# Kernel tuning notes

Measured on AMD Instinct MI355X. Metric: run time of the kernel, lower is better.

Reference implementation:

```python
import jax, jax.numpy as jnp
import numpy as np

# Hyperparameters (DetectionLoss __init__ defaults)
ALPHA = 0.75
GAMMA = 2.0
NUM_NEG = 10000
NUM_HARD = 100
NEG_POS_RATIO = 100
FN_WEIGHT = 4.0
FN_THRESHOLD = 0.8
HFP_T1 = 0.5
HFP_T2 = 0.7
HFP_W1 = 1.5
HFP_W2 = 2.0

B, N = 16, 884736  # batch, num anchor points (96^3 crop)


def setup_inputs() -> dict:
    key = jax.random.key(0)
    kp, kt, km = jax.random.split(key, 3)
    pred = jax.random.normal(kp, (B, N, 1), dtype=jnp.float32)
    # sparse binary positive targets (~440 positives per sample)
    target = (jax.random.uniform(kt, (B, N, 1)) < 5e-4).astype(jnp.float32)
    mask_ignore = (jax.random.uniform(km, (B, N, 1)) < 1e-2).astype(jnp.float32)
    mask_ignore = mask_ignore * (1.0 - target)
    return {"pred": pred, "target": target, "mask_ignore": mask_ignore}


def _bce_with_logits(x, t):
    # numerically stable binary_cross_entropy_with_logits, reduction='none'
    return jnp.maximum(x, 0.0) - x * t + jnp.log1p(jnp.exp(-jnp.abs(x)))


def _cls_loss(pred, target, mask_ignore):
    b = pred.shape[0]
    pred = pred.reshape(b, -1)
    target = target.reshape(b, -1)
    mask_ignore = mask_ignore.reshape(b, -1)
    # fixed keys replace python random.sample for negative subsampling
    keys = jax.random.split(jax.random.key(42), b)

    def per_sample(pred_b, target_b, mask_b, key):
        is_pos = target_b == 1.0
        is_neg = target_b == 0.0
        cls_prob = jnp.clip(jax.nn.sigmoid(jax.lax.stop_gradient(pred_b)), 1e-4, 1.0 - 1e-4)
        alpha_factor = jnp.where(is_pos, ALPHA, 1.0 - ALPHA)
        focal_w = alpha_factor * jnp.where(is_pos, 1.0 - cls_prob, cls_prob) ** GAMMA
        loss = jnp.where(mask_b == 0.0, focal_w * _bce_with_logits(pred_b, target_b), 0.0)
        npos = jnp.sum(is_pos)
        # false-negative upweight (only positive points qualify, so it is a
        # no-op in the npos==0 branch, matching the torch control flow)
        loss = loss * jnp.where((cls_prob < FN_THRESHOLD) & is_pos, FN_WEIGHT, 1.0)
        # hard false-positive upweight (applied in both branches)
        hfp_w = HFP_W1 + jnp.clip((cls_prob - HFP_T1) / (HFP_T2 - HFP_T1), 0.0, 1.0) * (HFP_W2 - HFP_W1)
        loss = loss * jnp.where((cls_prob > HFP_T1) & is_neg, hfp_w, 1.0)
        pos_loss = jnp.sum(jnp.where(is_pos, loss, 0.0))
        # random subsample of NUM_NEG negatives without replacement:
        # top-NUM_NEG by uniform random score restricted to negatives
        rnd = jax.random.uniform(key, pred_b.shape)
        sample_score = jnp.where(is_neg, rnd, -jnp.inf)
        _, idx = jax.lax.top_k(sample_score, NUM_NEG)
        neg_losses = jnp.where(is_neg[idx], loss[idx], 0.0)
        # hard-negative mining: keep top-k of the sampled negative losses
        topv = jax.lax.top_k(neg_losses, NUM_NEG)[0]
        k = jnp.where(npos > 0, jnp.minimum(NEG_POS_RATIO * npos, NUM_NEG), NUM_HARD)
        neg_sum = jnp.sum(jnp.where(jnp.arange(NUM_NEG) < k, topv, 0.0))
        # pos branch divides both sums by npos; neg branch divides by 1
        denom = jnp.where(npos > 0, jnp.maximum(npos.astype(pred_b.dtype), 1.0), 1.0)
        return pos_loss / denom, neg_sum / denom

    pos, neg = jax.vmap(per_sample)(pred, target, mask_ignore, keys)
    cls_pos_loss = jnp.sum(pos) / b
    cls_neg_loss = jnp.sum(neg) / b
    return jnp.stack([cls_pos_loss, cls_neg_loss])


def reference(pred, target, mask_ignore):
    return _cls_loss(pred, target, mask_ignore)
```

## Files before the change

kernel.cpp:

```cpp
#include <hip/hip_runtime.h>
#include <stdint.h>


#define BATCH 16
#define NPTS 884736u
#define THRESH_KEY 8266976u
#define THRESH_W   4232691712u
#define KEYMAX 8388607u
#define KSEL 10000u
#define TLO 8285746u
#define THI 8301746u
#define TLO_W 4242301952u
#define HI_W  4250494464u
#define WCAP 3072u
#define SCAP 160
#define BCAP 64
#define NBLK 432u
#define EPT 8u
#define HDRB 512


struct KeyPairs { unsigned k[2 * BATCH]; };

__host__ __device__ __forceinline__ void tf2x32(unsigned k0, unsigned k1,
                                                unsigned x0, unsigned x1,
                                                unsigned& o0, unsigned& o1)
{
  unsigned ks0 = k0, ks1 = k1, ks2 = k0 ^ k1 ^ 0x1BD11BDAu;
  x0 += ks0; x1 += ks1;
#define TF_R(r) { x0 += x1; x1 = __builtin_rotateleft32(x1, r); x1 ^= x0; }
  TF_R(13) TF_R(15) TF_R(26) TF_R(6)
  x0 += ks1; x1 += ks2 + 1u;
  TF_R(17) TF_R(29) TF_R(16) TF_R(24)
  x0 += ks2; x1 += ks0 + 2u;
  TF_R(13) TF_R(15) TF_R(26) TF_R(6)
  x0 += ks0; x1 += ks1 + 3u;
  TF_R(17) TF_R(29) TF_R(16) TF_R(24)
  x0 += ks1; x1 += ks2 + 4u;
  TF_R(13) TF_R(15) TF_R(26) TF_R(6)
  x0 += ks2; x1 += ks0 + 5u;
#undef TF_R
  o0 = x0; o1 = x1;
}

__device__ __forceinline__ float lossf(float x, float t, float m)
{
  float e  = __expf(-x);
  float p  = __fdividef(1.0f, 1.0f + e);
  p = fminf(fmaxf(p, 1e-4f), 1.0f - 1e-4f);
  bool is_pos = (t == 1.0f);
  float alpha = is_pos ? 0.75f : 0.25f;
  float pw = is_pos ? (1.0f - p) : p;
  float soft = __logf(1.0f + __expf(-fabsf(x)));
  float bce = fmaxf(x, 0.0f) - x * t + soft;
  float L = (m == 0.0f) ? alpha * pw * pw * bce : 0.0f;
  if (is_pos && p < 0.8f) L *= 4.0f;
  if (!is_pos && p > 0.5f)
    L *= 1.5f + fminf(fmaxf((p - 0.5f) * 5.0f, 0.0f), 1.0f) * 0.5f;
  return L;
}

__global__ __launch_bounds__(256) void mono(
    const float* __restrict__ pred, const float* __restrict__ target,
    const float* __restrict__ mask, char* __restrict__ hdr,
    unsigned* __restrict__ wkey, unsigned* __restrict__ widx,
    float* __restrict__ wloss, KeyPairs kp)
{
  const int b = blockIdx.y;
  const int tid = threadIdx.x;
  const unsigned i0 = (blockIdx.x * 256u + tid) * EPT;
  const size_t sbase = (size_t)b * NPTS;
  const size_t off = sbase + i0;
  const unsigned k0 = kp.k[2 * b], k1 = kp.k[2 * b + 1];
  char* line = hdr + (size_t)b * HDRB;

  __shared__ unsigned s_n, s_nhi, s_npos;
  __shared__ float    s_psum, s_hsum;
  __shared__ unsigned s_si[SCAP], s_skey[SCAP];

  if (tid == 0) { s_n = 0; s_nhi = 0; s_npos = 0; s_psum = 0.0f; s_hsum = 0.0f; }
  __syncthreads();

  float4 t4a = *reinterpret_cast<const float4*>(target + off);
  float4 t4b = *reinterpret_cast<const float4*>(target + off + 4);
  float tv[8] = { t4a.x, t4a.y, t4a.z, t4a.w, t4b.x, t4b.y, t4b.z, t4b.w };

  unsigned kw[8];
#pragma unroll
  for (int r = 0; r < 8; ++r) {
    unsigned o0, o1;
    tf2x32(k0, k1, 0u, i0 + (unsigned)r, o0, o1);
    kw[r] = o0 ^ o1;
  }

  unsigned posm = 0, him = 0, winm = 0;
#pragma unroll
  for (int r = 0; r < 8; ++r) {
    bool c  = (tv[r] == 0.0f) && (kw[r] >= THRESH_W);
    bool hi = c && (kw[r] >= HI_W);
    bool wn = c && !hi && (kw[r] >= TLO_W);
    him   |= (unsigned)hi << r;
    winm  |= (unsigned)wn << r;
    posm  |= (unsigned)(tv[r] == 1.0f) << r;
  }

  const unsigned flags = him | winm | posm;
  if (flags) {
    unsigned nf = (unsigned)__popc(flags);
    unsigned base = atomicAdd(&s_n, nf);
    unsigned j = 0;
#pragma unroll
    for (int r = 0; r < 8; ++r) {
      if ((flags >> r) & 1u) {
        unsigned cls = ((posm >> r) & 1u) ? 2u : (((winm >> r) & 1u) ? 1u : 0u);
        unsigned p = base + j; ++j;
        if (p < SCAP) {
          s_si[p] = (i0 + (unsigned)r) | (cls << 20);
          s_skey[p] = kw[r] >> 9;
        } else {
          float x = pred[off + r], m = mask[off + r];
          float L = lossf(x, (cls == 2u) ? 1.0f : 0.0f, m);
          if (cls == 2u) { atomicAdd(&s_psum, L); atomicAdd(&s_npos, 1u); }
          else if (cls == 0u) { atomicAdd(&s_hsum, L); atomicAdd(&s_nhi, 1u); }
          else {
            unsigned g = atomicAdd((unsigned*)(line + 192), 1u);
            if (g < WCAP) {
              wkey[b * WCAP + g] = kw[r] >> 9;
              widx[b * WCAP + g] = i0 + (unsigned)r;
              wloss[b * WCAP + g] = L;
            } else atomicOr((unsigned*)(line + 196), 1u);
          }
        }
      }
    }
  }
  __syncthreads();

  const unsigned n = s_n < SCAP ? s_n : SCAP;
  unsigned rec = (tid < (int)n) ? s_si[tid] : 0u;
  unsigned cls = (tid < (int)n) ? (rec >> 20) : 3u;
  unsigned i = rec & 0xFFFFFu;
  float L = 0.0f;
  if (cls < 3u) {
    float x = pred[sbase + i], m = mask[sbase + i];
    L = lossf(x, (cls == 2u) ? 1.0f : 0.0f, m);
  }
  if (cls == 2u) { atomicAdd(&s_psum, L); atomicAdd(&s_npos, 1u); }
  else if (cls == 0u) { atomicAdd(&s_hsum, L); atomicAdd(&s_nhi, 1u); }
  {
    bool isw = (cls == 1u);
    unsigned long long mv = __ballot(isw ? 1 : 0);
    if (isw) {
      int lane = tid & 63;
      unsigned rank = (unsigned)__popcll(mv & ((1ull << lane) - 1ull));
      int leader = __ffsll((unsigned long long)mv) - 1;
      unsigned gb = 0;
      if (lane == leader)
        gb = atomicAdd((unsigned*)(line + 192), (unsigned)__popcll(mv));
      gb = __shfl(gb, leader, 64);
      unsigned g = gb + rank;
      if (g < WCAP) {
        wkey[b * WCAP + g] = s_skey[tid];
        widx[b * WCAP + g] = i;
        wloss[b * WCAP + g] = L;
      } else atomicOr((unsigned*)(line + 196), 1u);
    }
  }
  __syncthreads();

  if (tid == 0) {
    if (s_nhi) { atomicAdd((unsigned*)(line + 128), s_nhi); atomicAdd((float*)(line + 132), s_hsum); }
    if (s_npos) { atomicAdd((unsigned*)(line + 4), s_npos); atomicAdd((float*)(line + 0), s_psum); }
  }
}

__global__ __launch_bounds__(256) void select_k(
    const float* __restrict__ pred, const float* __restrict__ target,
    const float* __restrict__ mask, char* __restrict__ hdr,
    const unsigned* __restrict__ wkey, const unsigned* __restrict__ widx,
    const float* __restrict__ wloss, float* __restrict__ out, KeyPairs kp)
{
  const int b = blockIdx.x;
  const int tid = threadIdx.x;
  char* line = hdr + (size_t)b * HDRB;
  unsigned* gticket = (unsigned*)(hdr + (size_t)BATCH * HDRB - 4);

  __shared__ unsigned skey[WCAP], sidx[WCAP];
  __shared__ float    sls[WCAP];
  __shared__ unsigned redu[256];
  __shared__ float    redf[256];
  __shared__ unsigned s_eqc, s_u1, s_tick;
  __shared__ unsigned s_eqi[BCAP];
  __shared__ float    s_eql[BCAP];
  __shared__ float    s_f;

  const unsigned n_hi   = *(const unsigned*)(line + 128);
  const float    sum_hi = *(const float*)(line + 132);
  const unsigned n_win  = *(const unsigned*)(line + 192);
  const unsigned fail   = *(const unsigned*)(line + 196);
  const unsigned npos   = *(const unsigned*)(line + 4);
  const unsigned k = (npos > 0u) ? ((100u * npos < KSEL) ? 100u * npos : KSEL) : 100u;
  const bool bad = fail || (n_hi > KSEL) || (n_hi + n_win < KSEL) ||
                   (n_win > WCAP) || (k < KSEL);

  auto redSumU = [&](unsigned v) -> unsigned {
    redu[tid] = v; __syncthreads();
    for (int s = 128; s > 0; s >>= 1) { if (tid < s) redu[tid] += redu[tid + s]; __syncthreads(); }
    unsigned r = redu[0]; __syncthreads(); return r;
  };
  auto redSumF = [&](float v) -> float {
    redf[tid] = v; __syncthreads();
    for (int s = 128; s > 0; s >>= 1) { if (tid < s) redf[tid] += redf[tid + s]; __syncthreads(); }
    float r = redf[0]; __syncthreads(); return r;
  };

  float res = 0.0f;

  if (!bad) {
    const unsigned nw = n_win;
    for (unsigned e = tid; e < nw; e += 256) {
      skey[e] = wkey[b * WCAP + e];
      sidx[e] = widx[b * WCAP + e];
      sls[e]  = wloss[b * WCAP + e];
    }
    __syncthreads();
    const unsigned need = KSEL - n_hi;
    if (need == 0) res = sum_hi;
    else {
      auto cGe = [&](unsigned v) -> unsigned {
        unsigned c = 0;
        for (unsigned e = tid; e < nw; e += 256) c += (skey[e] >= v) ? 1u : 0u;
        return redSumU(c);
      };
      unsigned lo = TLO, hi = THI;
      while (lo < hi) {
        unsigned mid = lo + (hi - lo + 1u) / 2u;
        if (cGe(mid) >= need) lo = mid; else hi = mid - 1u;
      }
      const unsigned V = lo;
      const unsigned c_gt = cGe(V + 1u);
      const unsigned m = need - c_gt;
      float s = 0.0f;
      for (unsigned e = tid; e < nw; e += 256) if (skey[e] > V) s += sls[e];
      float sum_gt = redSumF(s);
      if (tid == 0) s_eqc = 0;
      __syncthreads();
      for (unsigned e = tid; e < nw; e += 256) {
        if (skey[e] == V) {
          unsigned p = atomicAdd(&s_eqc, 1u);
          if (p < BCAP) { s_eqi[p] = sidx[e]; s_eql[p] = sls[e]; }
        }
      }
      __syncthreads();
      if (tid == 0) {
        unsigned ne = s_eqc; if (ne > BCAP) ne = BCAP;
        unsigned mm = (m < ne) ? m : ne;
        float es = 0.0f;
        for (unsigned a = 0; a < mm; ++a) {
          unsigned best = a;
          for (unsigned q = a + 1; q < ne; ++q)
            if (s_eqi[q] < s_eqi[best]) best = q;
          unsigned ti = s_eqi[a]; s_eqi[a] = s_eqi[best]; s_eqi[best] = ti;
          float tl = s_eql[a]; s_eql[a] = s_eql[best]; s_eql[best] = tl;
          es += s_eql[a];
        }
        s_f = sum_hi + sum_gt + es;
      }
      __syncthreads();
      res = s_f;
    }
  } else {
    const float* T = target + (size_t)b * NPTS;
    const float* P = pred   + (size_t)b * NPTS;
    const float* M = mask   + (size_t)b * NPTS;
    const unsigned k0 = kp.k[2 * b], k1 = kp.k[2 * b + 1];
    auto keyOf = [&](unsigned i) -> unsigned {
      unsigned o0, o1; tf2x32(k0, k1, 0u, i, o0, o1); return (o0 ^ o1) >> 9;
    };
    auto cKeyGe = [&](unsigned v) -> unsigned {
      unsigned c = 0;
      for (unsigned i = tid; i < NPTS; i += 256)
        if (T[i] == 0.0f && keyOf(i) >= v) c++;
      return redSumU(c);
    };
    const unsigned cnt = cKeyGe(THRESH_KEY);
    const bool take_all = (cnt <= KSEL);
    const unsigned nsel = take_all ? cnt : KSEL;
    unsigned V = 0, idxcut = 0xffffffffu; float eq_sum = 0.0f;
    if (!take_all) {
      unsigned lo = THRESH_KEY, hi = KEYMAX;
      while (lo < hi) {
        unsigned mid = lo + (hi - lo + 1u) / 2u;
        if (cKeyGe(mid) >= KSEL) lo = mid; else hi = mid - 1u;
      }
      V = lo;
      unsigned c_gt = cKeyGe(V + 1u);
      unsigned needq = KSEL - c_gt;
      if (tid == 0) s_eqc = 0;
      __syncthreads();
      for (unsigned i = tid; i < NPTS; i += 256)
        if (T[i] == 0.0f && keyOf(i) == V) {
          unsigned p = atomicAdd(&s_eqc, 1u);
          if (p < BCAP) s_eqi[p] = i;
        }
      __syncthreads();
      if (tid == 0) {
        unsigned ne = s_eqc; if (ne > BCAP) ne = BCAP;
        unsigned mm = (needq < ne) ? needq : ne;
        float es = 0.0f; unsigned ic = 0xffffffffu;
        for (unsigned a = 0; a < mm; ++a) {
          unsigned best = a;
          for (unsigned q = a + 1; q < ne; ++q)
            if (s_eqi[q] < s_eqi[best]) best = q;
          unsigned ti = s_eqi[a]; s_eqi[a] = s_eqi[best]; s_eqi[best] = ti;
          es += lossf(P[s_eqi[a]], 0.0f, M[s_eqi[a]]);
        }
        if (mm > 0) ic = s_eqi[mm - 1];
        s_f = es; s_u1 = ic;
      }
      __syncthreads();
      eq_sum = s_f; idxcut = s_u1;
      __syncthreads();
    }
    if (k >= nsel) {
      float s = 0.0f;
      for (unsigned i = tid; i < NPTS; i += 256) {
        if (T[i] != 0.0f) continue;
        unsigned kk = keyOf(i);
        if (kk < THRESH_KEY) continue;
        if (take_all || kk > V) s += lossf(P[i], 0.0f, M[i]);
      }
      res = redSumF(s) + (take_all ? 0.0f : eq_sum);
    } else {
      auto cLossGe = [&](unsigned w) -> unsigned {
        unsigned c = 0;
        for (unsigned i = tid; i < NPTS; i += 256) {
          if (T[i] != 0.0f) continue;
          unsigned kk = keyOf(i);
          if (kk < THRESH_KEY) continue;
          bool sel = take_all || kk > V || (kk == V && i <= idxcut);
          if (sel && __float_as_uint(lossf(P[i], 0.0f, M[i])) >= w) c++;
        }
        return redSumU(c);
      };
      unsigned lo = 0u, hi = 0x7f7fffffu;
      while (lo < hi) {
        unsigned mid = lo + (hi - lo + 1u) / 2u;
        if (cLossGe(mid) >= k) lo = mid; else hi = mid - 1u;
      }
      unsigned cgt = cLossGe(lo + 1u);
      float s = 0.0f;
      for (unsigned i = tid; i < NPTS; i += 256) {
        if (T[i] != 0.0f) continue;
        unsigned kk = keyOf(i);
        if (kk < THRESH_KEY) continue;
        bool sel = take_all || kk > V || (kk == V && i <= idxcut);
        float L = lossf(P[i], 0.0f, M[i]);
        if (sel && __float_as_uint(L) > lo) s += L;
      }
      res = redSumF(s) + (float)(k - cgt) * __uint_as_float(lo);
    }
  }

  if (tid == 0) {
    atomicExch((float*)(line + 256), res);
    __threadfence();
    s_tick = atomicAdd(gticket, 1u);
  }
  __syncthreads();
  if (s_tick == BATCH - 1) {
    float ps = 0.0f, ns = 0.0f;
    if (tid < BATCH) {
      char* ln = hdr + (size_t)tid * HDRB;
      float pp = atomicAdd((float*)(ln + 0), 0.0f);
      unsigned np = atomicAdd((unsigned*)(ln + 4), 0u);
      float nr = atomicAdd((float*)(ln + 256), 0.0f);
      float denom = (np > 0u) ? fmaxf((float)np, 1.0f) : 1.0f;
      ps = pp / denom;
      ns = nr / denom;
    }
#pragma unroll
    for (int s = 8; s > 0; s >>= 1) {
      ps += __shfl_down(ps, s, 64);
      ns += __shfl_down(ns, s, 64);
    }
    if (tid == 0) {
      out[0] = ps / (float)BATCH;
      out[1] = ns / (float)BATCH;
    }
  }
}

extern "C" void kernel_launch(void* const* d_in, const int* in_sizes, int n_in,
                              void* d_out, int out_size, void* d_ws, size_t ws_size,
                              hipStream_t stream)
{
  const float* pred   = (const float*)d_in[0];
  const float* target = (const float*)d_in[1];
  const float* mask   = (const float*)d_in[2];
  float* out = (float*)d_out;

  const size_t HDRSZ = (size_t)BATCH * HDRB;
  const size_t FIXED = HDRSZ + 3 * (size_t)BATCH * WCAP * 4;
  if (ws_size < FIXED || out_size < 2) {
    hipMemsetAsync(d_out, 0, sizeof(float) * (out_size > 0 ? out_size : 1), stream);
    return;
  }

  char* ws = (char*)d_ws;
  char*     hdr   = ws;
  unsigned* wkey  = (unsigned*)(ws + HDRSZ);
  unsigned* widx  = wkey + (size_t)BATCH * WCAP;
  float*    wloss = (float*)(widx + (size_t)BATCH * WCAP);

  KeyPairs kp;
  for (unsigned b = 0; b < BATCH; ++b) {
    unsigned o0, o1;
    tf2x32(0u, 42u, 0u, b, o0, o1);
    kp.k[2 * b] = o0; kp.k[2 * b + 1] = o1;
  }

  hipMemsetAsync(hdr, 0, HDRSZ, stream);

  mono<<<dim3(NBLK, BATCH), 256, 0, stream>>>(pred, target, mask, hdr,
                                              wkey, widx, wloss, kp);
  select_k<<<BATCH, 256, 0, stream>>>(pred, target, mask, hdr,
                                      wkey, widx, wloss, out, kp);
}
```

Before: 75.79 us.

## Replace global atomics and memset with per-block partials and a prefix-sum compaction

Each mono block now handles 16 elements per thread, using half as many blocks. It writes its counts and sums to a per-block partial slot and keeps window candidates in a fixed per-block buffer, so it no longer does global atomics on per-sample header lines. select_k reduces the partials and builds the window array with a shared-memory prefix scan. This removes the hipMemsetAsync launch and global atomic contention. The ticket is reset inside mono, and a per-block cap of 40 window entries could push some samples onto the slow fallback path.

```diff
diff --git a/kernel.cpp b/kernel.cpp
--- a/kernel.cpp
+++ b/kernel.cpp
@@ -13,12 +13,16 @@
 #define TLO_W 4242301952u
 #define HI_W  4250494464u
 #define WCAP 3072u
-#define SCAP 160
+#define WBCAP 40u
+#define SCAP 192
 #define BCAP 64
-#define NBLK 432u
-#define EPT 8u
+#define NBLK2 216u
+#define EPT 16u
 #define HDRB 512
 
+#define OFF_PART 8192
+#define PARTN (NBLK2 * BATCH)
+#define OFF_WIN (OFF_PART + 5 * PARTN * 4)
 
 struct KeyPairs { unsigned k[2 * BATCH]; };
 
@@ -62,73 +66,88 @@
 
 __global__ __launch_bounds__(256) void mono(
     const float* __restrict__ pred, const float* __restrict__ target,
-    const float* __restrict__ mask, char* __restrict__ hdr,
-    unsigned* __restrict__ wkey, unsigned* __restrict__ widx,
-    float* __restrict__ wloss, KeyPairs kp)
+    const float* __restrict__ mask, char* __restrict__ ws, KeyPairs kp)
 {
   const int b = blockIdx.y;
   const int tid = threadIdx.x;
-  const unsigned i0 = (blockIdx.x * 256u + tid) * EPT;
+  const unsigned blk = blockIdx.x;
+  const unsigned rb = (unsigned)b * NBLK2 + blk;
+  const unsigned i0 = (blk * 256u + tid) * EPT;
   const size_t sbase = (size_t)b * NPTS;
-  const size_t off = sbase + i0;
   const unsigned k0 = kp.k[2 * b], k1 = kp.k[2 * b + 1];
-  char* line = hdr + (size_t)b * HDRB;
-
-  __shared__ unsigned s_n, s_nhi, s_npos;
+
+  unsigned* p_nhi  = (unsigned*)(ws + OFF_PART);
+  unsigned* p_hsum = p_nhi + PARTN;
+  unsigned* p_npos = p_hsum + PARTN;
+  unsigned* p_psum = p_npos + PARTN;
+  unsigned* p_nwin = p_psum + PARTN;
+  unsigned* wkeyg  = (unsigned*)(ws + OFF_WIN);
+  unsigned* widxg  = wkeyg + (size_t)PARTN * WBCAP;
+  float*    wlossg = (float*)(widxg + (size_t)PARTN * WBCAP);
+
+  if (b == 0 && blk == 0 && tid == 0)
+    *(unsigned*)(ws + 8188) = 0u;
+
+  __shared__ unsigned s_n, s_nhi, s_npos, s_wn, s_fail;
   __shared__ float    s_psum, s_hsum;
   __shared__ unsigned s_si[SCAP], s_skey[SCAP];
 
-  if (tid == 0) { s_n = 0; s_nhi = 0; s_npos = 0; s_psum = 0.0f; s_hsum = 0.0f; }
+  if (tid == 0) { s_n = 0; s_nhi = 0; s_npos = 0; s_wn = 0; s_fail = 0;
+                  s_psum = 0.0f; s_hsum = 0.0f; }
   __syncthreads();
 
-  float4 t4a = *reinterpret_cast<const float4*>(target + off);
-  float4 t4b = *reinterpret_cast<const float4*>(target + off + 4);
-  float tv[8] = { t4a.x, t4a.y, t4a.z, t4a.w, t4b.x, t4b.y, t4b.z, t4b.w };
-
-  unsigned kw[8];
 #pragma unroll
-  for (int r = 0; r < 8; ++r) {
-    unsigned o0, o1;
-    tf2x32(k0, k1, 0u, i0 + (unsigned)r, o0, o1);
-    kw[r] = o0 ^ o1;
-  }
-
-  unsigned posm = 0, him = 0, winm = 0;
-#pragma unroll
-  for (int r = 0; r < 8; ++r) {
-    bool c  = (tv[r] == 0.0f) && (kw[r] >= THRESH_W);
-    bool hi = c && (kw[r] >= HI_W);
-    bool wn = c && !hi && (kw[r] >= TLO_W);
-    him   |= (unsigned)hi << r;
-    winm  |= (unsigned)wn << r;
-    posm  |= (unsigned)(tv[r] == 1.0f) << r;
-  }
-
-  const unsigned flags = him | winm | posm;
-  if (flags) {
-    unsigned nf = (unsigned)__popc(flags);
-    unsigned base = atomicAdd(&s_n, nf);
-    unsigned j = 0;
+  for (int h = 0; h < 2; ++h) {
+    const unsigned ib = i0 + (unsigned)h * 8u;
+    const size_t off = sbase + ib;
+    float4 t4a = *reinterpret_cast<const float4*>(target + off);
+    float4 t4b = *reinterpret_cast<const float4*>(target + off + 4);
+    float tv[8] = { t4a.x, t4a.y, t4a.z, t4a.w, t4b.x, t4b.y, t4b.z, t4b.w };
+
+    unsigned kw[8];
 #pragma unroll
     for (int r = 0; r < 8; ++r) {
-      if ((flags >> r) & 1u) {
-        unsigned cls = ((posm >> r) & 1u) ? 2u : (((winm >> r) & 1u) ? 1u : 0u);
-        unsigned p = base + j; ++j;
-        if (p < SCAP) {
-          s_si[p] = (i0 + (unsigned)r) | (cls << 20);
-          s_skey[p] = kw[r] >> 9;
-        } else {
-          float x = pred[off + r], m = mask[off + r];
-          float L = lossf(x, (cls == 2u) ? 1.0f : 0.0f, m);
-          if (cls == 2u) { atomicAdd(&s_psum, L); atomicAdd(&s_npos, 1u); }
-          else if (cls == 0u) { atomicAdd(&s_hsum, L); atomicAdd(&s_nhi, 1u); }
-          else {
-            unsigned g = atomicAdd((unsigned*)(line + 192), 1u);
-            if (g < WCAP) {
-              wkey[b * WCAP + g] = kw[r] >> 9;
-              widx[b * WCAP + g] = i0 + (unsigned)r;
-              wloss[b * WCAP + g] = L;
-            } else atomicOr((unsigned*)(line + 196), 1u);
+      unsigned o0, o1;
+      tf2x32(k0, k1, 0u, ib + (unsigned)r, o0, o1);
+      kw[r] = o0 ^ o1;
+    }
+
+    unsigned posm = 0, him = 0, winm = 0;
+#pragma unroll
+    for (int r = 0; r < 8; ++r) {
+      bool c  = (tv[r] == 0.0f) && (kw[r] >= THRESH_W);
+      bool hi = c && (kw[r] >= HI_W);
+      bool wn = c && !hi && (kw[r] >= TLO_W);
+      him  |= (unsigned)hi << r;
+      winm |= (unsigned)wn << r;
+      posm |= (unsigned)(tv[r] == 1.0f) << r;
+    }
+
+    const unsigned flags = him | winm | posm;
+    if (flags) {
+      unsigned nf = (unsigned)__popc(flags);
+      unsigned base = atomicAdd(&s_n, nf);
+      unsigned j = 0;
+#pragma unroll
+      for (int r = 0; r < 8; ++r) {
+        if ((flags >> r) & 1u) {
+          unsigned cls = ((posm >> r) & 1u) ? 2u : (((winm >> r) & 1u) ? 1u : 0u);
+          unsigned p = base + j; ++j;
+          if (p < SCAP) {
+            s_si[p] = (ib + (unsigned)r) | (cls << 20);
+            s_skey[p] = kw[r] >> 9;
+          } else {
+            float x = pred[off + r], m = mask[off + r];
+            float L = lossf(x, (cls == 2u) ? 1.0f : 0.0f, m);
+            if (cls == 2u) { atomicAdd(&s_psum, L); atomicAdd(&s_npos, 1u); }
+            else if (cls == 0u) { atomicAdd(&s_hsum, L); atomicAdd(&s_nhi, 1u); }
+            else {
+              unsigned g = atomicAdd(&s_wn, 1u);
+              if (g < WBCAP) {
+                size_t o = (size_t)rb * WBCAP + g;
+                wkeyg[o] = kw[r] >> 9; widxg[o] = ib + (unsigned)r; wlossg[o] = L;
+              } else atomicOr(&s_fail, 1u);
+            }
           }
         }
       }
@@ -147,61 +166,54 @@
   }
   if (cls == 2u) { atomicAdd(&s_psum, L); atomicAdd(&s_npos, 1u); }
   else if (cls == 0u) { atomicAdd(&s_hsum, L); atomicAdd(&s_nhi, 1u); }
-  {
-    bool isw = (cls == 1u);
-    unsigned long long mv = __ballot(isw ? 1 : 0);
-    if (isw) {
-      int lane = tid & 63;
-      unsigned rank = (unsigned)__popcll(mv & ((1ull << lane) - 1ull));
-      int leader = __ffsll((unsigned long long)mv) - 1;
-      unsigned gb = 0;
-      if (lane == leader)
-        gb = atomicAdd((unsigned*)(line + 192), (unsigned)__popcll(mv));
-      gb = __shfl(gb, leader, 64);
-      unsigned g = gb + rank;
-      if (g < WCAP) {
-        wkey[b * WCAP + g] = s_skey[tid];
-        widx[b * WCAP + g] = i;
-        wloss[b * WCAP + g] = L;
-      } else atomicOr((unsigned*)(line + 196), 1u);
-    }
+  else if (cls == 1u) {
+    unsigned g = atomicAdd(&s_wn, 1u);
+    if (g < WBCAP) {
+      size_t o = (size_t)rb * WBCAP + g;
+      wkeyg[o] = s_skey[tid]; widxg[o] = i; wlossg[o] = L;
+    } else atomicOr(&s_fail, 1u);
   }
   __syncthreads();
 
   if (tid == 0) {
-    if (s_nhi) { atomicAdd((unsigned*)(line + 128), s_nhi); atomicAdd((float*)(line + 132), s_hsum); }
-    if (s_npos) { atomicAdd((unsigned*)(line + 4), s_npos); atomicAdd((float*)(line + 0), s_psum); }
+    p_nhi[rb]  = s_nhi;
+    p_hsum[rb] = __float_as_uint(s_hsum);
+    p_npos[rb] = s_npos;
+    p_psum[rb] = __float_as_uint(s_psum);
+    unsigned wn = s_wn;
+    unsigned fail = (s_fail || wn > WBCAP) ? 0x80000000u : 0u;
+    p_nwin[rb] = (wn < WBCAP ? wn : WBCAP) | fail;
   }
 }
 
 __global__ __launch_bounds__(256) void select_k(
     const float* __restrict__ pred, const float* __restrict__ target,
-    const float* __restrict__ mask, char* __restrict__ hdr,
-    const unsigned* __restrict__ wkey, const unsigned* __restrict__ widx,
-    const float* __restrict__ wloss, float* __restrict__ out, KeyPairs kp)
+    const float* __restrict__ mask, char* __restrict__ ws,
+    float* __restrict__ out, KeyPairs kp)
 {
   const int b = blockIdx.x;
   const int tid = threadIdx.x;
-  char* line = hdr + (size_t)b * HDRB;
-  unsigned* gticket = (unsigned*)(hdr + (size_t)BATCH * HDRB - 4);
+  char* line = ws + (size_t)b * HDRB;
+  unsigned* gticket = (unsigned*)(ws + 8188);
+
+  const unsigned* p_nhi  = (const unsigned*)(ws + OFF_PART);
+  const unsigned* p_hsum = p_nhi + PARTN;
+  const unsigned* p_npos = p_hsum + PARTN;
+  const unsigned* p_psum = p_npos + PARTN;
+  const unsigned* p_nwin = p_psum + PARTN;
+  const unsigned* wkeyg  = (const unsigned*)(ws + OFF_WIN);
+  const unsigned* widxg  = wkeyg + (size_t)PARTN * WBCAP;
+  const float*    wlossg = (const float*)(widxg + (size_t)PARTN * WBCAP);
 
   __shared__ unsigned skey[WCAP], sidx[WCAP];
   __shared__ float    sls[WCAP];
+  __shared__ unsigned sc[256];
   __shared__ unsigned redu[256];
   __shared__ float    redf[256];
   __shared__ unsigned s_eqc, s_u1, s_tick;
   __shared__ unsigned s_eqi[BCAP];
   __shared__ float    s_eql[BCAP];
   __shared__ float    s_f;
-
-  const unsigned n_hi   = *(const unsigned*)(line + 128);
-  const float    sum_hi = *(const float*)(line + 132);
-  const unsigned n_win  = *(const unsigned*)(line + 192);
-  const unsigned fail   = *(const unsigned*)(line + 196);
-  const unsigned npos   = *(const unsigned*)(line + 4);
-  const unsigned k = (npos > 0u) ? ((100u * npos < KSEL) ? 100u * npos : KSEL) : 100u;
-  const bool bad = fail || (n_hi > KSEL) || (n_hi + n_win < KSEL) ||
-                   (n_win > WCAP) || (k < KSEL);
 
   auto redSumU = [&](unsigned v) -> unsigned {
     redu[tid] = v; __syncthreads();
@@ -214,14 +226,48 @@
     float r = redf[0]; __syncthreads(); return r;
   };
 
+  unsigned mynhi = 0, mynpos = 0, mycnt = 0, myfail = 0;
+  float myh = 0.0f, myp = 0.0f;
+  unsigned myrb = (unsigned)b * NBLK2 + (unsigned)tid;
+  if (tid < (int)NBLK2) {
+    mynhi = p_nhi[myrb];
+    myh   = __uint_as_float(p_hsum[myrb]);
+    mynpos = p_npos[myrb];
+    myp   = __uint_as_float(p_psum[myrb]);
+    unsigned w = p_nwin[myrb];
+    mycnt = w & 0x7FFFFFFFu;
+    myfail = w >> 31;
+  }
+  const unsigned n_hi = redSumU(mynhi);
+  const float sum_hi = redSumF(myh);
+  const unsigned npos = redSumU(mynpos);
+  const float pos_sum = redSumF(myp);
+  const unsigned failN = redSumU(myfail);
+
+  sc[tid] = mycnt; __syncthreads();
+  for (int s = 1; s < 256; s <<= 1) {
+    unsigned v = (tid >= s) ? sc[tid - s] : 0u;
+    __syncthreads();
+    sc[tid] += v;
+    __syncthreads();
+  }
+  const unsigned nw = sc[255];
+  const unsigned wbase = sc[tid] - mycnt;
+
+  const unsigned k = (npos > 0u) ? ((100u * npos < KSEL) ? 100u * npos : KSEL) : 100u;
+  const bool bad = failN || (n_hi > KSEL) || (n_hi + nw < KSEL) ||
+                   (nw > WCAP) || (k < KSEL);
+
   float res = 0.0f;
 
   if (!bad) {
-    const unsigned nw = n_win;
-    for (unsigned e = tid; e < nw; e += 256) {
-      skey[e] = wkey[b * WCAP + e];
-      sidx[e] = widx[b * WCAP + e];
-      sls[e]  = wloss[b * WCAP + e];
+    if (tid < (int)NBLK2) {
+      size_t src = (size_t)myrb * WBCAP;
+      for (unsigned e = 0; e < mycnt; ++e) {
+        skey[wbase + e] = wkeyg[src + e];
+        sidx[wbase + e] = widxg[src + e];
+        sls[wbase + e]  = wlossg[src + e];
+      }
     }
     __syncthreads();
     const unsigned need = KSEL - n_hi;
@@ -363,6 +409,8 @@
   }
 
   if (tid == 0) {
+    atomicExch((float*)(line + 0), pos_sum);
+    atomicExch((unsigned*)(line + 4), npos);
     atomicExch((float*)(line + 256), res);
     __threadfence();
     s_tick = atomicAdd(gticket, 1u);
@@ -371,7 +419,7 @@
   if (s_tick == BATCH - 1) {
     float ps = 0.0f, ns = 0.0f;
     if (tid < BATCH) {
-      char* ln = hdr + (size_t)tid * HDRB;
+      char* ln = ws + (size_t)tid * HDRB;
       float pp = atomicAdd((float*)(ln + 0), 0.0f);
       unsigned np = atomicAdd((unsigned*)(ln + 4), 0u);
       float nr = atomicAdd((float*)(ln + 256), 0.0f);
@@ -400,18 +448,13 @@
   const float* mask   = (const float*)d_in[2];
   float* out = (float*)d_out;
 
-  const size_t HDRSZ = (size_t)BATCH * HDRB;
-  const size_t FIXED = HDRSZ + 3 * (size_t)BATCH * WCAP * 4;
+  const size_t FIXED = OFF_WIN + 3 * (size_t)PARTN * WBCAP * 4;
   if (ws_size < FIXED || out_size < 2) {
     hipMemsetAsync(d_out, 0, sizeof(float) * (out_size > 0 ? out_size : 1), stream);
     return;
   }
 
   char* ws = (char*)d_ws;
-  char*     hdr   = ws;
-  unsigned* wkey  = (unsigned*)(ws + HDRSZ);
-  unsigned* widx  = wkey + (size_t)BATCH * WCAP;
-  float*    wloss = (float*)(widx + (size_t)BATCH * WCAP);
 
   KeyPairs kp;
   for (unsigned b = 0; b < BATCH; ++b) {
@@ -420,10 +463,6 @@
     kp.k[2 * b] = o0; kp.k[2 * b + 1] = o1;
   }
 
-  hipMemsetAsync(hdr, 0, HDRSZ, stream);
-
-  mono<<<dim3(NBLK, BATCH), 256, 0, stream>>>(pred, target, mask, hdr,
-                                              wkey, widx, wloss, kp);
-  select_k<<<BATCH, 256, 0, stream>>>(pred, target, mask, hdr,
-                                      wkey, widx, wloss, out, kp);
+  mono<<<dim3(NBLK2, BATCH), 256, 0, stream>>>(pred, target, mask, ws, kp);
+  select_k<<<BATCH, 256, 0, stream>>>(pred, target, mask, ws, out, kp);
 }
```

Result: faster. 68.29 us (-9.9%).
